# Kernel tuning notes

Hardware: AMD Instinct MI355X
Metric: run time of the kernel (lower is better)

## Reference

```python
import jax, jax.numpy as jnp
import numpy as np

NUM_CLASSES = 80
STRIDES = (32, 16, 8)
SCORE_THRESH = 0.01
NMS_THRESH = 0.45
TOP_K = 200
PRE_K = 4096          # pre-NMS candidate cap (greedy NMS only ever emits TOP_K boxes)
NEG = -1e9            # 'suppressed' score sentinel (avoids -inf NaN issues)
CLS_OFFSET = 4096.0   # class-aware NMS: offset boxes per class (boxes live in [0, 608])

_ANCHORS_PX = [[(116, 90), (156, 198), (373, 326)],
               [(30, 61), (62, 45), (59, 119)],
               [(10, 13), (16, 30), (33, 23)]]


def setup_inputs() -> dict:
    key = jax.random.key(0)
    bs, img = 8, 608
    inp = {}
    for lvl, (stride, anc) in enumerate(zip(STRIDES, _ANCHORS_PX)):
        H = W = img // stride
        key, k = jax.random.split(key)
        inp[f"in{lvl}"] = jax.random.normal(k, (bs, 3 * (NUM_CLASSES + 5), H, W), dtype=jnp.float32)
        aw = jnp.array([a[0] / stride for a in anc], jnp.float32)
        ah = jnp.array([a[1] / stride for a in anc], jnp.float32)
        inp[f"aw{lvl}"] = jnp.broadcast_to(aw[None, :, None, None], (bs, 3, H, W))
        inp[f"ah{lvl}"] = jnp.broadcast_to(ah[None, :, None, None], (bs, 3, H, W))
        inp[f"gx{lvl}"] = jnp.broadcast_to(jnp.arange(W, dtype=jnp.float32)[None, None, None, :], (bs, 3, H, W))
        inp[f"gy{lvl}"] = jnp.broadcast_to(jnp.arange(H, dtype=jnp.float32)[None, None, :, None], (bs, 3, H, W))
    return inp


def _decode_level(x, aw, ah, gx, gy, stride):
    bs, _, H, W = x.shape
    x = x.reshape(bs, -1, NUM_CLASSES + 5, H, W).transpose(0, 1, 3, 4, 2)  # [bs,3,H,W,85]
    px = jax.nn.sigmoid(x[..., 0]) + gx
    py = jax.nn.sigmoid(x[..., 1]) + gy
    pw = jnp.exp(x[..., 2]) * aw
    ph = jnp.exp(x[..., 3]) * ah
    conf = jax.nn.sigmoid(x[..., 4])
    cls = jax.nn.sigmoid(x[..., 5:])
    boxes = jnp.stack([px, py, pw, ph], -1) * jnp.float32(stride)  # [bs,3,H,W,4] (cx,cy,w,h)
    return boxes.reshape(bs, -1, 4), conf.reshape(bs, -1), cls.reshape(bs, -1, NUM_CLASSES)


def _center_to_corner(b):
    cx, cy, w, h = b[..., 0], b[..., 1], b[..., 2], b[..., 3]
    return jnp.stack([cx - w / 2, cy - h / 2, cx + w / 2, cy + h / 2], -1)


def _nms_image(boxes, conf, cls):
    # boxes [N,4] corner, conf [N], cls [N,C]
    N, C = cls.shape
    scores = (conf[:, None] * cls).reshape(-1)                          # [N*C]
    cboxes = jnp.broadcast_to(boxes[:, None, :], (N, C, 4)).reshape(-1, 4)
    labels = jnp.broadcast_to(jnp.arange(C), (N, C)).reshape(-1)
    s = jnp.where(scores > SCORE_THRESH, scores, NEG)
    top_s, idx = jax.lax.top_k(s, PRE_K)
    b = cboxes[idx]                                                     # [PRE_K,4]
    l = labels[idx]
    ob = b + (l.astype(jnp.float32) * CLS_OFFSET)[:, None]              # class-aware offset
    area = (ob[:, 2] - ob[:, 0]) * (ob[:, 3] - ob[:, 1])

    def step(live, _):
        i = jnp.argmax(live)
        si, bi, ai = live[i], ob[i], area[i]
        x1 = jnp.maximum(bi[0], ob[:, 0]); y1 = jnp.maximum(bi[1], ob[:, 1])
        x2 = jnp.minimum(bi[2], ob[:, 2]); y2 = jnp.minimum(bi[3], ob[:, 3])
        inter = jnp.clip(x2 - x1, 0.0) * jnp.clip(y2 - y1, 0.0)
        iou = inter / (ai + area - inter + 1e-9)
        live = jnp.where(iou > NMS_THRESH, NEG, live)                   # suppresses self too
        return live, (i, si)

    _, (sel, sel_s) = jax.lax.scan(step, top_s, None, length=TOP_K)
    valid = sel_s > SCORE_THRESH
    out_b = jnp.where(valid[:, None], b[sel], 0.0)
    out_l = jnp.where(valid, l[sel], 0).astype(jnp.float32)
    out_s = jnp.where(valid, sel_s, 0.0)
    return jnp.concatenate([out_b, out_l[:, None], out_s[:, None]], -1)  # [TOP_K, 6]


def _forward(levels):
    boxes, conf, cls = [], [], []
    for (x, aw, ah, gx, gy), stride in zip(levels, STRIDES):
        bb, cc, cl = _decode_level(x, aw, ah, gx, gy, stride)
        boxes.append(bb); conf.append(cc); cls.append(cl)
    boxes = _center_to_corner(jnp.concatenate(boxes, 1))   # [bs,N,4]
    conf = jnp.concatenate(conf, 1)                        # [bs,N]
    cls = jnp.concatenate(cls, 1)                          # [bs,N,C]
    return jax.vmap(_nms_image)(boxes, conf, cls)          # [bs,TOP_K,6]


def reference(in0, aw0, ah0, gx0, gy0, in1, aw1, ah1, gx1, gy1, in2, aw2, ah2, gx2, gy2):
    levels = [(in0, aw0, ah0, gx0, gy0), (in1, aw1, ah1, gx1, gy1), (in2, aw2, ah2, gx2, gy2)]
    return _forward(levels)
```

## Files before the change

### kernel.cpp

```cpp
#include <hip/hip_runtime.h>
#include <stdint.h>

typedef unsigned int u32;
typedef unsigned long long u64;

#define NCLS 80
#define NBOX 22743
#define PREK 4096
#define BCAP 65536
#define NIMG 8
#define SCORE_TH 0.01f
#define IOU_TH 0.45f
#define TOPK 200

#define DCH 20
#define DNCH 4
#define GCH 10
#define GNCH 8

#define LCAP 1536

#define BKCAP 8
#define HCAP 224
#define HUGE_TH 3488.0f

#define RJC 4
#define RJW 1024

#define HIST_OFF 0
#define META_OFF 131072
#define CNT_OFF  131200
#define ZERO_BYTES 133248
#define WIN_OFF  133248
#define BND_OFF  395392
#define PART_OFF BND_OFF
#define BOX_OFF  4589696
#define SKEY_OFF 7500800
#define SOBOX_OFF 7762944
#define SAREA_OFF 8287232

__device__ __forceinline__ float sigmf(float x) { return 1.0f / (1.0f + expf(-x)); }

#define BIN_BASE 61440u

__device__ __forceinline__ u64 pad_key(int i) { return (u64)(~(u32)i); }

__global__ __launch_bounds__(256) void decode_hist_all(const float* __restrict__ in0,
                              const float* __restrict__ in1, const float* __restrict__ in2,
                              float4* __restrict__ boxes, u32* __restrict__ hist) {
  __shared__ u32 lh[4096];
  const int img = blockIdx.y;
  const int c0 = blockIdx.z * DCH;
  for (int i = threadIdx.x; i < 4096; i += 256) lh[i] = 0;
  __syncthreads();

  const int bx = blockIdx.x;
  if (bx < 5) {
    const int W = 19, HW = 361;
    const int r = bx * 256 + threadIdx.x;
    if (r < 3 * HW) {
      const int a = r / HW, p = r - a * HW;
      const int y = p / W, x = p - y * W;
      const float* base = in0 + ((size_t)(img * 255 + a * 85)) * (size_t)HW + p;
      float l[DCH];
#pragma unroll
      for (int k = 0; k < DCH; ++k) l[k] = base[(size_t)(5 + c0 + k) * HW];
      const float x4 = base[4 * (size_t)HW];
      if (c0 == 0) {
        const float aw = (a == 0) ? 3.625f : ((a == 1) ? 4.875f : 11.65625f);
        const float ah = (a == 0) ? 2.8125f : ((a == 1) ? 6.1875f : 10.1875f);
        const float x0 = base[0];
        const float x1 = base[(size_t)HW];
        const float x2 = base[2 * (size_t)HW];
        const float x3 = base[3 * (size_t)HW];
        const float px = sigmf(x0) + (float)x;
        const float py = sigmf(x1) + (float)y;
        const float pw = expf(x2) * aw;
        const float ph = expf(x3) * ah;
        const float cx = px * 32.f, cy = py * 32.f, bw = pw * 32.f, bh = ph * 32.f;
        boxes[(size_t)img * NBOX + r] =
            make_float4(cx - bw * 0.5f, cy - bh * 0.5f, cx + bw * 0.5f, cy + bh * 0.5f);
      }
      const float conf = sigmf(x4);
      if (conf > SCORE_TH) {
#pragma unroll
        for (int k = 0; k < DCH; ++k) {
          float s = conf * sigmf(l[k]);
          if (s > SCORE_TH) {
            u32 bin = (__float_as_uint(s) >> 14) - BIN_BASE;
            atomicAdd(&lh[bin], 1u);
          }
        }
      }
    }
  } else {
    const bool L1 = bx < 10;
    const float* in = L1 ? in1 : in2;
    const int W = L1 ? 38 : 76;
    const int HW = L1 ? 1444 : 5776;
    const int lvl_off = L1 ? 1083 : 5415;
    const float stride = L1 ? 16.f : 8.f;
    const int HW4 = HW >> 2;
    const int idx = (bx - (L1 ? 5 : 10)) * 256 + threadIdx.x;
    if (idx < 3 * HW4) {
      const int a = idx / HW4;
      const int p0 = (idx - a * HW4) << 2;
      const float* base = in + ((size_t)(img * 255 + a * 85)) * (size_t)HW + p0;
      float4 scv[DCH];
#pragma unroll
      for (int k = 0; k < DCH; ++k)
        scv[k] = *(const float4*)(base + (size_t)(5 + c0 + k) * HW);
      float4 v4 = *(const float4*)(base + 4 * (size_t)HW);
      const float* t4 = (const float*)&v4;
      float conf[4];
      if (c0 == 0) {
        const float aw = L1 ? ((a == 0) ? 1.875f : ((a == 1) ? 3.875f : 3.6875f))
                            : ((a == 0) ? 1.25f : ((a == 1) ? 2.f : 4.125f));
        const float ah = L1 ? ((a == 0) ? 3.8125f : ((a == 1) ? 2.8125f : 7.4375f))
                            : ((a == 0) ? 1.625f : ((a == 1) ? 3.75f : 2.875f));
        float4 v0 = *(const float4*)(base);
        float4 v1 = *(const float4*)(base + (size_t)HW);
        float4 v2 = *(const float4*)(base + 2 * (size_t)HW);
        float4 v3 = *(const float4*)(base + 3 * (size_t)HW);
        const float* t0 = (const float*)&v0;
        const float* t1 = (const float*)&v1;
        const float* t2 = (const float*)&v2;
        const float* t3 = (const float*)&v3;
        float4* bout = boxes + (size_t)img * NBOX + lvl_off + a * HW + p0;
#pragma unroll
        for (int i = 0; i < 4; ++i) {
          const int p = p0 + i;
          const int y = p / W, x = p - y * W;
          const float px = sigmf(t0[i]) + (float)x;
          const float py = sigmf(t1[i]) + (float)y;
          const float pw = expf(t2[i]) * aw;
          const float ph = expf(t3[i]) * ah;
          const float cx = px * stride, cy = py * stride, bw = pw * stride, bh = ph * stride;
          bout[i] = make_float4(cx - bw * 0.5f, cy - bh * 0.5f, cx + bw * 0.5f, cy + bh * 0.5f);
        }
      }
#pragma unroll
      for (int i = 0; i < 4; ++i) conf[i] = sigmf(t4[i]);
#pragma unroll
      for (int k = 0; k < DCH; ++k) {
        const float* s4 = (const float*)&scv[k];
#pragma unroll
        for (int i = 0; i < 4; ++i) {
          float s = conf[i] * sigmf(s4[i]);
          if (s > SCORE_TH) {
            u32 bin = (__float_as_uint(s) >> 14) - BIN_BASE;
            atomicAdd(&lh[bin], 1u);
          }
        }
      }
    }
  }
  __syncthreads();
  u32* gh = hist + (size_t)img * 4096;
  for (int i = threadIdx.x; i < 4096; i += 256) {
    u32 v = lh[i];
    if (v) atomicAdd(&gh[i], v);
  }
}

__global__ void scan_k(const u32* __restrict__ hist, int* __restrict__ meta) {
  const int img = blockIdx.x;
  const u32* h = hist + (size_t)img * 4096;
  __shared__ u32 lsum[256];
  __shared__ u32 above[256];
  __shared__ u32 s_total;
  const int t = threadIdx.x;
  u32 s = 0;
  for (int j = 0; j < 16; ++j) s += h[t * 16 + j];
  lsum[t] = s;
  __syncthreads();
  if (t == 0) {
    u32 acc = 0;
    for (int i = 255; i >= 0; --i) { above[i] = acc; acc += lsum[i]; }
    s_total = acc;
  }
  __syncthreads();
  const u32 K = PREK;
  int* m = meta + img * 4;
  if (s_total < K) {
    if (t == 0) { m[0] = -1; m[1] = 0; }
  } else {
    if (above[t] < K && above[t] + lsum[t] >= K) {
      u32 cum = above[t];
      for (int j = 15; j >= 0; --j) {
        u32 hv = h[t * 16 + j];
        cum += hv;
        if (cum >= K) { m[0] = t * 16 + j; m[1] = (int)(K - (cum - hv)); break; }
      }
    }
  }
}

__device__ __forceinline__ void flush_list(const u64* llist, int lcnt, int cap,
                                           int* gctr, u64* glist, int gcap) {
  __shared__ int gbase_s;
  int n = lcnt < cap ? lcnt : cap;
  if (threadIdx.x == 0) gbase_s = n ? atomicAdd(gctr, n) : 0;
  __syncthreads();
  const int gb = gbase_s;
  for (int i = threadIdx.x; i < n; i += 256) {
    int pos = gb + i;
    if (pos < gcap) glist[pos] = llist[i];
  }
}

__global__ __launch_bounds__(256) void gather_all(const float* __restrict__ in0,
                         const float* __restrict__ in1, const float* __restrict__ in2,
                         const int* __restrict__ meta, int* __restrict__ cnt,
                         u64* __restrict__ winners, u64* __restrict__ boundary) {
  __shared__ u64 lwin[LCAP];
  __shared__ u64 lbnd[LCAP];
  __shared__ int lwc, lbc;
  const int img = blockIdx.y;
  const int c0 = blockIdx.z * GCH;
  if (threadIdx.x == 0) { lwc = 0; lbc = 0; }
  __syncthreads();

  const int B = meta[img * 4 + 0];
  int* cw = &cnt[img * 64];
  int* cb = &cnt[img * 64 + 32];
  u64* wl = winners + (size_t)img * PREK;
  u64* bl = boundary + (size_t)img * BCAP;
  const int bx = blockIdx.x;

  if (bx < 5) {
    const int HW = 361;
    const int r = bx * 256 + threadIdx.x;
    if (r < 3 * HW) {
      const int a = r / HW, p = r - a * HW;
      const float* base = in0 + ((size_t)(img * 255 + a * 85)) * (size_t)HW + p;
      const int boxg = r;
      float l[GCH];
#pragma unroll
      for (int k = 0; k < GCH; ++k) l[k] = base[(size_t)(5 + c0 + k) * HW];
      const float conf = sigmf(base[4 * (size_t)HW]);
#pragma unroll
      for (int k = 0; k < GCH; ++k) {
        float s = conf * sigmf(l[k]);
        if (s > SCORE_TH) {
          u32 key = __float_as_uint(s);
          int wbin = (int)((key >> 14) - BIN_BASE);
          if (wbin >= B) {
            u64 kv = ((u64)key << 32) | (u64)(~(u32)(boxg * NCLS + (c0 + k)));
            if (wbin > B) {
              int p2 = atomicAdd(&lwc, 1);
              if (p2 < LCAP) lwin[p2] = kv;
              else { int g = atomicAdd(cw, 1); if (g < PREK) wl[g] = kv; }
            } else {
              int p2 = atomicAdd(&lbc, 1);
              if (p2 < LCAP) lbnd[p2] = kv;
              else { int g = atomicAdd(cb, 1); if (g < BCAP) bl[g] = kv; }
            }
          }
        }
      }
    }
  } else {
    const bool L1 = bx < 10;
    const float* in = L1 ? in1 : in2;
    const int HW = L1 ? 1444 : 5776;
    const int lvl_off = L1 ? 1083 : 5415;
    const int HW4 = HW >> 2;
    const int idx = (bx - (L1 ? 5 : 10)) * 256 + threadIdx.x;
    if (idx < 3 * HW4) {
      const int a = idx / HW4;
      const int p0 = (idx - a * HW4) << 2;
      const float* base = in + ((size_t)(img * 255 + a * 85)) * (size_t)HW + p0;
      const int boxg0 = lvl_off + a * HW + p0;
      float4 scv[GCH];
#pragma unroll
      for (int k = 0; k < GCH; ++k)
        scv[k] = *(const float4*)(base + (size_t)(5 + c0 + k) * HW);
      float4 v4 = *(const float4*)(base + 4 * (size_t)HW);
      const float* t4 = (const float*)&v4;
      float conf[4];
#pragma unroll
      for (int i = 0; i < 4; ++i) conf[i] = sigmf(t4[i]);
#pragma unroll
      for (int k = 0; k < GCH; ++k) {
        const float* s4 = (const float*)&scv[k];
        const int c = c0 + k;
#pragma unroll
        for (int i = 0; i < 4; ++i) {
          float s = conf[i] * sigmf(s4[i]);
          if (s > SCORE_TH) {
            u32 key = __float_as_uint(s);
            int wbin = (int)((key >> 14) - BIN_BASE);
            if (wbin >= B) {
              u64 kv = ((u64)key << 32) | (u64)(~(u32)((boxg0 + i) * NCLS + c));
              if (wbin > B) {
                int p = atomicAdd(&lwc, 1);
                if (p < LCAP) lwin[p] = kv;
                else { int g = atomicAdd(cw, 1); if (g < PREK) wl[g] = kv; }
              } else {
                int p = atomicAdd(&lbc, 1);
                if (p < LCAP) lbnd[p] = kv;
                else { int g = atomicAdd(cb, 1); if (g < BCAP) bl[g] = kv; }
              }
            }
          }
        }
      }
    }
  }
  __syncthreads();
  flush_list(lwin, lwc, LCAP, cw, wl, PREK);
  flush_list(lbnd, lbc, LCAP, cb, bl, BCAP);
}

__global__ void resolve_k(const u64* __restrict__ boundary, const int* __restrict__ meta,
                          int* __restrict__ cnt, u64* __restrict__ winners) {
  const int img = blockIdx.x;
  const int T = meta[img * 4 + 1];
  int bc = cnt[img * 64 + 32];
  if (bc > BCAP) bc = BCAP;
  if (T <= 0 || bc <= 0) return;
  const u64* bnd = boundary + (size_t)img * BCAP;
  u64* wl = winners + (size_t)img * PREK;
  int* cw = &cnt[img * 64];

  __shared__ u32 h2[16384];
  __shared__ u32 lsum[256];
  __shared__ u32 above[256];
  __shared__ u32 s_total;
  __shared__ int sB2, sT2;
  __shared__ u64 ties[512];
  __shared__ int tcnt;
  __shared__ u64 lw2[PREK];
  __shared__ int lw2c;
  __shared__ int gbase_s;
  const int t = threadIdx.x;
  for (int i = t; i < 16384; i += 256) h2[i] = 0;
  if (t == 0) { tcnt = 0; sB2 = -1; sT2 = 0; lw2c = 0; }
  __syncthreads();
  for (int i = t; i < bc; i += 256) atomicAdd(&h2[(u32)(bnd[i] >> 32) & 0x3FFFu], 1u);
  __syncthreads();
  u32 s = 0;
  for (int j = 0; j < 64; ++j) s += h2[t * 64 + j];
  lsum[t] = s;
  __syncthreads();
  if (t == 0) {
    u32 acc = 0;
    for (int i = 255; i >= 0; --i) { above[i] = acc; acc += lsum[i]; }
    s_total = acc;
  }
  __syncthreads();
  if ((int)s_total > T) {
    if (above[t] < (u32)T && above[t] + lsum[t] >= (u32)T) {
      u32 cum = above[t];
      for (int j = 63; j >= 0; --j) {
        u32 hv = h2[t * 64 + j];
        cum += hv;
        if (cum >= (u32)T) { sB2 = t * 64 + j; sT2 = (int)((u32)T - (cum - hv)); break; }
      }
    }
  }
  __syncthreads();
  const int B2 = sB2, T2 = sT2;
  for (int i = t; i < bc; i += 256) {
    u64 e = bnd[i];
    int low = (int)((u32)(e >> 32) & 0x3FFFu);
    if (low > B2) {
      int p = atomicAdd(&lw2c, 1);
      if (p < PREK) lw2[p] = e;
    } else if (low == B2) {
      int tp = atomicAdd(&tcnt, 1);
      if (tp < 512) ties[tp] = e;
    }
  }
  __syncthreads();
  int n = lw2c < PREK ? lw2c : PREK;
  if (t == 0) gbase_s = n ? atomicAdd(cw, n) : 0;
  __syncthreads();
  for (int i = t; i < n; i += 256) {
    int pos = gbase_s + i;
    if (pos < PREK) wl[pos] = lw2[i];
  }
  __syncthreads();
  if (t == 0 && T2 > 0) {
    int tc = tcnt < 512 ? tcnt : 512;
    for (int k = 0; k < T2 && k < tc; ++k) {
      int bi = -1; u64 bk = 0;
      for (int i = 0; i < tc; ++i)
        if (ties[i] > bk) { bk = ties[i]; bi = i; }
      if (bi < 0) break;
      ties[bi] = 0;
      int pos = atomicAdd(cw, 1);
      if (pos < PREK) wl[pos] = bk;
    }
  }
}

__global__ __launch_bounds__(256) void rank_part_k(const u64* __restrict__ winners,
                                                   const int* __restrict__ cnt,
                                                   int* __restrict__ part) {
  __shared__ u64 lk[RJW];
  const int img = blockIdx.y;
  const int kc = blockIdx.x >> 2;
  const int jc = blockIdx.x & 3;
  const int t = threadIdx.x;
  int wc = cnt[img * 64]; if (wc > PREK) wc = PREK;
  const u64* wl = winners + (size_t)img * PREK;
  for (int i = t; i < RJW; i += 256) {
    const int gj = jc * RJW + i;
    lk[i] = (gj < wc) ? wl[gj] : pad_key(gj);
  }
  __syncthreads();
  const int ki_idx = kc * 256 + t;
  const u64 ki = (ki_idx < wc) ? wl[ki_idx] : pad_key(ki_idx);
  int rank = 0;
#pragma unroll 8
  for (int j = 0; j < RJW; ++j) rank += (lk[j] > ki) ? 1 : 0;
  part[(((size_t)img * RJC) + jc) * PREK + ki_idx] = rank;
}

__global__ __launch_bounds__(256) void rank_scatter_k(const u64* __restrict__ winners,
                                              const int* __restrict__ cnt,
                                              const int* __restrict__ part,
                                              const float4* __restrict__ boxes,
                                              u64* __restrict__ skey,
                                              float4* __restrict__ sobox,
                                              float* __restrict__ sarea) {
  const int img = blockIdx.y;
  const int i = blockIdx.x * 256 + threadIdx.x;
  int wc = cnt[img * 64]; if (wc > PREK) wc = PREK;
  const u64* wl = winners + (size_t)img * PREK;
  const u64 ki = (i < wc) ? wl[i] : pad_key(i);
  const int* pb = part + (size_t)img * RJC * PREK + i;
  int rank = pb[0] + pb[PREK] + pb[2 * PREK] + pb[3 * PREK];
  skey[(size_t)img * PREK + rank] = ki;
  if (i < wc) {
    u32 ridx = ~(u32)ki;
    int c = (int)(ridx % NCLS);
    int bi = (int)(ridx / NCLS);
    float4 b = boxes[(size_t)img * NBOX + bi];
    float off = 4096.0f * (float)c;
    float4 ob = make_float4(b.x + off, b.y + off, b.z + off, b.w + off);
    sobox[(size_t)img * PREK + rank] = ob;
    sarea[(size_t)img * PREK + rank] = (ob.z - ob.x) * (ob.w - ob.y);
  } else {
    sobox[(size_t)img * PREK + rank] = make_float4(0.f, 0.f, 0.f, 0.f);
    sarea[(size_t)img * PREK + rank] = 0.f;
  }
}

__global__ __launch_bounds__(64) void scan_nms_k(const u64* __restrict__ skey,
                                                 const float4* __restrict__ sobox,
                                                 const float* __restrict__ sarea,
                                                 float* __restrict__ out) {
  __shared__ float4 bxc[NCLS][BKCAP];
  __shared__ float  arc[NCLS][BKCAP];
  __shared__ int    cntc[NCLS];
  __shared__ float4 bxa[TOPK];
  __shared__ float  ara[TOPK];
  __shared__ float4 bxh[HCAP];
  __shared__ float  arh[HCAP];
  __shared__ int    nhuge_s;
  __shared__ float4 chb[64];
  __shared__ float  cha[64];
  const int img = blockIdx.x;
  const int lane = threadIdx.x;
  float* orow = out + (size_t)img * (TOPK * 6);
  for (int i = lane; i < TOPK * 6; i += 64) orow[i] = 0.f;
  for (int i = lane; i < NCLS; i += 64) cntc[i] = 0;
  if (lane == 0) nhuge_s = 0;
  const u64* K = skey + (size_t)img * PREK;
  const float4* Bp = sobox + (size_t)img * PREK;
  const float* Ap = sarea + (size_t)img * PREK;
  int nsel = 0;
  for (int chunk = 0; chunk < PREK / 64 && nsel < TOPK; ++chunk) {
    const int j = chunk * 64 + lane;
    const u64 kj = K[j];
    const float score = __uint_as_float((u32)(kj >> 32));
    bool alive = (score > SCORE_TH);
    if (__ballot(alive) == 0ull) break;
    const float4 ob = Bp[j];
    const float ar = Ap[j];
    const u32 ridx = ~(u32)kj;
    const int myc = (int)(ridx % NCLS);
    const bool huge = (ob.z - ob.x > HUGE_TH) || (ob.w - ob.y > HUGE_TH);
    chb[lane] = ob; cha[lane] = ar;

    {
      const int n0 = cntc[myc];
      const int n = n0 < BKCAP ? n0 : BKCAP;
      for (int k = 0; __ballot(alive && k < n) != 0ull; k += 2) {
        const int k0 = (k < BKCAP - 1) ? k : (BKCAP - 1);
        const int k1 = (k + 1 < BKCAP - 1) ? (k + 1) : (BKCAP - 1);
        const float4 b0 = bxc[myc][k0]; const float a0 = arc[myc][k0];
        const float4 b1 = bxc[myc][k1]; const float a1 = arc[myc][k1];
        if (alive && k < n) {
          float xx1 = fmaxf(b0.x, ob.x), yy1 = fmaxf(b0.y, ob.y);
          float xx2 = fminf(b0.z, ob.z), yy2 = fminf(b0.w, ob.w);
          float inter = fmaxf(xx2 - xx1, 0.f) * fmaxf(yy2 - yy1, 0.f);
          float iou = inter / (a0 + ar - inter + 1e-9f);
          if (iou > IOU_TH) alive = false;
        }
        if (alive && k + 1 < n) {
          float xx1 = fmaxf(b1.x, ob.x), yy1 = fmaxf(b1.y, ob.y);
          float xx2 = fminf(b1.z, ob.z), yy2 = fminf(b1.w, ob.w);
          float inter = fmaxf(xx2 - xx1, 0.f) * fmaxf(yy2 - yy1, 0.f);
          float iou = inter / (a1 + ar - inter + 1e-9f);
          if (iou > IOU_TH) alive = false;
        }
      }
    }
    {
      const int nh = nhuge_s;
      for (int k = 0; k < nh && __ballot(alive) != 0ull; k += 2) {
        const int k0 = (k < nh - 1) ? k : (nh - 1);
        const int k1 = (k + 1 < nh - 1) ? (k + 1) : (nh - 1);
        const float4 b0 = bxh[k0]; const float a0 = arh[k0];
        const float4 b1 = bxh[k1]; const float a1 = arh[k1];
        if (alive) {
          float xx1 = fmaxf(b0.x, ob.x), yy1 = fmaxf(b0.y, ob.y);
          float xx2 = fminf(b0.z, ob.z), yy2 = fminf(b0.w, ob.w);
          float inter = fmaxf(xx2 - xx1, 0.f) * fmaxf(yy2 - yy1, 0.f);
          float iou = inter / (a0 + ar - inter + 1e-9f);
          if (iou > IOU_TH) alive = false;
        }
        if (alive && k + 1 < nh) {
          float xx1 = fmaxf(b1.x, ob.x), yy1 = fmaxf(b1.y, ob.y);
          float xx2 = fminf(b1.z, ob.z), yy2 = fminf(b1.w, ob.w);
          float inter = fmaxf(xx2 - xx1, 0.f) * fmaxf(yy2 - yy1, 0.f);
          float iou = inter / (a1 + ar - inter + 1e-9f);
          if (iou > IOU_TH) alive = false;
        }
      }
    }
    if (__ballot(alive && huge) != 0ull) {
      const int na = nsel;
      for (int k = 0; k < na; k += 2) {
        const int k0 = (k < na - 1) ? k : (na - 1);
        const int k1 = (k + 1 < na - 1) ? (k + 1) : (na - 1);
        const float4 b0 = bxa[k0]; const float a0 = ara[k0];
        const float4 b1 = bxa[k1]; const float a1 = ara[k1];
        if (alive && huge) {
          float xx1 = fmaxf(b0.x, ob.x), yy1 = fmaxf(b0.y, ob.y);
          float xx2 = fminf(b0.z, ob.z), yy2 = fminf(b0.w, ob.w);
          float inter = fmaxf(xx2 - xx1, 0.f) * fmaxf(yy2 - yy1, 0.f);
          float iou = inter / (a0 + ar - inter + 1e-9f);
          if (iou > IOU_TH) alive = false;
        }
        if (alive && huge && k + 1 < na) {
          float xx1 = fmaxf(b1.x, ob.x), yy1 = fmaxf(b1.y, ob.y);
          float xx2 = fminf(b1.z, ob.z), yy2 = fminf(b1.w, ob.w);
          float inter = fmaxf(xx2 - xx1, 0.f) * fmaxf(yy2 - yy1, 0.f);
          float iou = inter / (a1 + ar - inter + 1e-9f);
          if (iou > IOU_TH) alive = false;
        }
        if (__ballot(alive && huge) == 0ull) break;
      }
    }
    u64 sup = 0ull;
#pragma unroll 4
    for (int jj = 0; jj < 64; ++jj) {
      const float4 bj = chb[jj];
      const float aj = cha[jj];
      float xx1 = fmaxf(bj.x, ob.x), yy1 = fmaxf(bj.y, ob.y);
      float xx2 = fminf(bj.z, ob.z), yy2 = fminf(bj.w, ob.w);
      float inter = fmaxf(xx2 - xx1, 0.f) * fmaxf(yy2 - yy1, 0.f);
      float iou = inter / (aj + ar - inter + 1e-9f);
      if (jj < lane && iou > IOU_TH) sup |= (1ull << jj);
    }
    u64 rem = __ballot(alive);
    u64 selbits = 0ull;
    while (rem != 0ull && nsel + (int)__popcll(selbits) < TOPK) {
      const int b = __builtin_ctzll(rem);
      selbits |= (1ull << b);
      rem &= ~(1ull << b);
      const u64 colb = __ballot((sup >> b) & 1ull);
      rem &= ~colb;
    }
    const bool selme = (selbits >> lane) & 1ull;
    if (selme) {
      const int slot = nsel + (int)__popcll(selbits & ((1ull << lane) - 1ull));
      bxa[slot] = ob; ara[slot] = ar;
      if (!huge) {
        int cc = atomicAdd(&cntc[myc], 1);
        if (cc < BKCAP) { bxc[myc][cc] = ob; arc[myc][cc] = ar; }
        else { int hn = atomicAdd(&nhuge_s, 1); if (hn < HCAP) { bxh[hn] = ob; arh[hn] = ar; } }
      } else {
        int hn = atomicAdd(&nhuge_s, 1);
        if (hn < HCAP) { bxh[hn] = ob; arh[hn] = ar; }
      }
      const float off = 4096.0f * (float)myc;
      orow[slot * 6 + 0] = ob.x - off;
      orow[slot * 6 + 1] = ob.y - off;
      orow[slot * 6 + 2] = ob.z - off;
      orow[slot * 6 + 3] = ob.w - off;
      orow[slot * 6 + 4] = (float)myc;
      orow[slot * 6 + 5] = score;
    }
    nsel += (int)__popcll(selbits);
  }
}

extern "C" void kernel_launch(void* const* d_in, const int* in_sizes, int n_in,
                              void* d_out, int out_size, void* d_ws, size_t ws_size,
                              hipStream_t stream) {
  const float* in0 = (const float*)d_in[0];
  const float* in1 = (const float*)d_in[5];
  const float* in2 = (const float*)d_in[10];
  char* ws = (char*)d_ws;
  u32* hist = (u32*)(ws + HIST_OFF);
  int* meta = (int*)(ws + META_OFF);
  int* cnt = (int*)(ws + CNT_OFF);
  u64* winners = (u64*)(ws + WIN_OFF);
  u64* boundary = (u64*)(ws + BND_OFF);
  int* part = (int*)(ws + PART_OFF);
  float4* boxes = (float4*)(ws + BOX_OFF);
  u64* skey = (u64*)(ws + SKEY_OFF);
  float4* sobox = (float4*)(ws + SOBOX_OFF);
  float* sarea = (float*)(ws + SAREA_OFF);
  float* out = (float*)d_out;

  hipMemsetAsync(d_ws, 0, ZERO_BYTES, stream);

  decode_hist_all<<<dim3(27, 8, DNCH), 256, 0, stream>>>(in0, in1, in2, boxes, hist);

  scan_k<<<8, 256, 0, stream>>>(hist, meta);

  gather_all<<<dim3(27, 8, GNCH), 256, 0, stream>>>(in0, in1, in2, meta, cnt, winners, boundary);

  resolve_k<<<8, 256, 0, stream>>>(boundary, meta, cnt, winners);

  rank_part_k<<<dim3(64, 8), 256, 0, stream>>>(winners, cnt, part);
  rank_scatter_k<<<dim3(16, 8), 256, 0, stream>>>(winners, cnt, part, boxes, skey, sobox, sarea);
  scan_nms_k<<<8, 64, 0, stream>>>(skey, sobox, sarea, out);
}
```

Measured before the change: 138.3 us.

## Prefetch next NMS chunk and restrict intra-chunk IoU to same-class/huge pairs

Register-prefetches the next 64-candidate chunk's key, box and area while the current chunk is processed, to hide global load latency in the serial NMS loop. Replaces the dense 64x64 intra-chunk IoU loop with a sparse loop over a per-lane mask of earlier, alive candidates sharing the same class (built from 7 ballots on class bits) or flagged huge. This skips pairs that cannot overlap because of the per-class coordinate offset. Because the sparse loop's trip count varies per lane, the wavefront now runs for as many iterations as its busiest lane.

```diff
diff --git a/kernel.cpp b/kernel.cpp
--- a/kernel.cpp
+++ b/kernel.cpp
@@ -473,18 +473,30 @@
   const float4* Bp = sobox + (size_t)img * PREK;
   const float* Ap = sarea + (size_t)img * PREK;
   int nsel = 0;
+  u64 kj = K[lane];
+  float4 ob = Bp[lane];
+  float ar = Ap[lane];
   for (int chunk = 0; chunk < PREK / 64 && nsel < TOPK; ++chunk) {
-    const int j = chunk * 64 + lane;
-    const u64 kj = K[j];
+    u64 kj_n = 0ull; float4 ob_n = make_float4(0.f, 0.f, 0.f, 0.f); float ar_n = 0.f;
+    if (chunk + 1 < PREK / 64) {
+      const int jn = (chunk + 1) * 64 + lane;
+      kj_n = K[jn]; ob_n = Bp[jn]; ar_n = Ap[jn];
+    }
     const float score = __uint_as_float((u32)(kj >> 32));
     bool alive = (score > SCORE_TH);
     if (__ballot(alive) == 0ull) break;
-    const float4 ob = Bp[j];
-    const float ar = Ap[j];
     const u32 ridx = ~(u32)kj;
     const int myc = (int)(ridx % NCLS);
     const bool huge = (ob.z - ob.x > HUGE_TH) || (ob.w - ob.y > HUGE_TH);
     chb[lane] = ob; cha[lane] = ar;
+
+    u64 mm = ~0ull;
+#pragma unroll
+    for (int k = 0; k < 7; ++k) {
+      const u64 bk = __ballot(((myc >> k) & 1) != 0);
+      mm &= (((myc >> k) & 1) != 0) ? bk : ~bk;
+    }
+    const u64 hb = __ballot(huge);
 
     {
       const int n0 = cntc[myc];
@@ -557,18 +569,22 @@
         if (__ballot(alive && huge) == 0ull) break;
       }
     }
+    const u64 amask = __ballot(alive);
+    const u64 below = (1ull << lane) - 1ull;
+    u64 tm = alive ? ((mm | hb | (huge ? ~0ull : 0ull)) & below & amask) : 0ull;
     u64 sup = 0ull;
-#pragma unroll 4
-    for (int jj = 0; jj < 64; ++jj) {
-      const float4 bj = chb[jj];
-      const float aj = cha[jj];
+    while (tm) {
+      const int t = (int)__builtin_ctzll(tm);
+      tm &= tm - 1ull;
+      const float4 bj = chb[t];
+      const float aj = cha[t];
       float xx1 = fmaxf(bj.x, ob.x), yy1 = fmaxf(bj.y, ob.y);
       float xx2 = fminf(bj.z, ob.z), yy2 = fminf(bj.w, ob.w);
       float inter = fmaxf(xx2 - xx1, 0.f) * fmaxf(yy2 - yy1, 0.f);
       float iou = inter / (aj + ar - inter + 1e-9f);
-      if (jj < lane && iou > IOU_TH) sup |= (1ull << jj);
-    }
-    u64 rem = __ballot(alive);
+      if (iou > IOU_TH) sup |= (1ull << t);
+    }
+    u64 rem = amask;
     u64 selbits = 0ull;
     while (rem != 0ull && nsel + (int)__popcll(selbits) < TOPK) {
       const int b = __builtin_ctzll(rem);
@@ -598,6 +614,7 @@
       orow[slot * 6 + 5] = score;
     }
     nsel += (int)__popcll(selbits);
+    kj = kj_n; ob = ob_n; ar = ar_n;
   }
 }
 
```

Result: faster. 117.1 us (-15.3%).
